# Kernel tuning notes

Measured on AMD Instinct MI355X. Metric: run time of the kernel, lower is better.

Reference implementation:

```python
import jax, jax.numpy as jnp
import numpy as np
from jax import lax

V, B, T, H = 16, 64, 256, 128  # num_variables, batch, seq_len, rnn_hidden_size
FC, C = 256, 10                # fc_hidden_size, num_classes


def setup_inputs() -> dict:
    key = jax.random.key(0)
    ks = jax.random.split(key, 8)
    s = 1.0 / np.sqrt(H)
    return {
        "x":   jax.random.normal(ks[0], (V, B, T, 1), jnp.float32),
        "Wih": jax.random.uniform(ks[1], (V, 3 * H, 1), jnp.float32, -s, s),
        "Whh": jax.random.uniform(ks[2], (V, 3 * H, H), jnp.float32, -s, s),
        "bih": jnp.zeros((V, 3 * H), jnp.float32),
        "bhh": jnp.zeros((V, 3 * H), jnp.float32),
        "Wp":  jax.random.normal(ks[3], (V, H), jnp.float32) * s,  # xavier-ish
        "bp":  jnp.zeros((V,), jnp.float32),
        "W1":  jax.random.normal(ks[4], (FC, V), jnp.float32) * (1.0 / np.sqrt(V)),
        "b1":  jnp.zeros((FC,), jnp.float32),
        "W2":  jax.random.normal(ks[5], (C, FC), jnp.float32) * (1.0 / np.sqrt(FC)),
        "b2":  jnp.zeros((C,), jnp.float32),
    }


def reference(x, Wih, Whh, bih, bhh, Wp, bp, W1, b1, W2, b2):
    # Batched multi-head GRU: all V independent heads scanned together.
    # Precompute input-side gates for all steps: [T, V, B, 3H]
    gi = jnp.einsum('vbti,vgi->tvbg', x, Wih) + bih[None, :, None, :]

    def step(h, gi_t):
        gh = jnp.einsum('vbh,vgh->vbg', h, Whh) + bhh[:, None, :]
        i_r, i_z, i_n = jnp.split(gi_t, 3, axis=-1)
        h_r, h_z, h_n = jnp.split(gh, 3, axis=-1)
        r = jax.nn.sigmoid(i_r + h_r)
        z = jax.nn.sigmoid(i_z + h_z)
        n = jnp.tanh(i_n + r * h_n)
        h_new = (1.0 - z) * n + z * h  # PyTorch GRU update
        return h_new, None

    h0 = jnp.zeros((x.shape[0], x.shape[1], Whh.shape[-1]), x.dtype)
    h_last, _ = lax.scan(step, h0, gi)  # [V, B, H] — last timestep hidden

    # per-variable Linear(H, 1), then concat over variables -> [B, V]
    concat = jnp.einsum('vbh,vh->bv', h_last, Wp) + bp[None, :]

    # Classifier: Linear -> ReLU -> Linear
    hfc = jax.nn.relu(concat @ W1.T + b1)
    return hfc @ W2.T + b2  # [B, C]
```

## Files before the change

### kernel.cpp

```cpp
#include <hip/hip_runtime.h>

#define NV  16
#define NB  64
#define NT  256
#define NH  128
#define NFC 256
#define NC  10

typedef _Float16 half8  __attribute__((ext_vector_type(8)));
typedef float    f32x4  __attribute__((ext_vector_type(4)));

__global__ __launch_bounds__(512, 2) void gru_scan_kernel(
    const float* __restrict__ x,   const float* __restrict__ Wih,
    const float* __restrict__ Whh, const float* __restrict__ bih,
    const float* __restrict__ bhh, const float* __restrict__ Wp,
    const float* __restrict__ bp,  float* __restrict__ concat_ws)
{
    __shared__ __align__(16) _Float16 frag[2][2048];
    __shared__ float xT[NT][5];
    __shared__ float pc[8][4];

    const int tid = threadIdx.x;
    const int w   = tid >> 6;
    const int l   = tid & 63;
    const int r   = l & 15;
    const int m4  = l >> 4;
    const int rb  = l & 3;
    const int s   = (l >> 2) & 3;
    const int bid = blockIdx.x;
    const int v   = bid >> 4;
    const int b0  = (bid & 15) << 2;
    const int j0  = (w << 4) + (m4 << 2);
    const int j   = j0 + s;

    constexpr float L2E = 1.44269504088896340736f;
    const float SCL0 = -L2E, SCL2 = 2.0f * L2E;

    {
        const int rr = tid >> 7;
        const int t0 = (tid & 127) << 1;
        const float2 xv = *(const float2*)(x + (size_t)(v * NB + b0 + rr) * NT + t0);
        xT[t0][rr] = xv.x; xT[t0 + 1][rr] = xv.y;
    }
    ((int4*)frag)[tid] = int4{0, 0, 0, 0};

    half8 afr[3][4];
    #pragma unroll
    for (int g = 0; g < 3; ++g) {
        const float sc = (g == 2) ? SCL2 : SCL0;
        #pragma unroll
        for (int kb = 0; kb < 4; ++kb) {
            const float* wpp = Whh + (size_t)(v * 384 + g * 128 + (w << 4) + r) * 128
                             + kb * 32 + m4 * 8;
            float4 lo = *(const float4*)wpp;
            float4 hi = *(const float4*)(wpp + 4);
            half8 hf;
            hf[0]=(_Float16)(sc*lo.x); hf[1]=(_Float16)(sc*lo.y);
            hf[2]=(_Float16)(sc*lo.z); hf[3]=(_Float16)(sc*lo.w);
            hf[4]=(_Float16)(sc*hi.x); hf[5]=(_Float16)(sc*hi.y);
            hf[6]=(_Float16)(sc*hi.z); hf[7]=(_Float16)(sc*hi.w);
            afr[g][kb] = hf;
        }
    }

    f32x4 c0i, c1i, c2i;
    #pragma unroll
    for (int q = 0; q < 4; ++q) {
        const int i0 = v * 384 + j0 + q;
        c0i[q] = SCL0 * (bhh[i0] + bih[i0]);
        c1i[q] = SCL0 * (bhh[i0 + 128] + bih[i0 + 128]);
        c2i[q] = SCL2 * bhh[i0 + 256];
    }
    const int ih = v * 384 + j;
    const float wih0 = SCL0 * Wih[ih];
    const float wih1 = SCL0 * Wih[ih + 128];
    const float wihn = SCL2 * Wih[ih + 256];
    const float bihn = SCL2 * bih[ih + 256];
    const float wpj  = Wp[v * NH + j];

    float h_old = 0.f;

    const int fwoff = (j >> 5) * 512 + (rb + 16 * ((j & 31) >> 3)) * 8 + (j & 7);
    const int rdoff = l * 8;

    __syncthreads();

    auto step = [&](const _Float16* __restrict__ fb, _Float16* __restrict__ fwb,
                    const float xr) {
        half8 bfr[4];
        #pragma unroll
        for (int kb = 0; kb < 4; ++kb)
            bfr[kb] = *(const half8*)(fb + kb * 512 + rdoff);

        f32x4 acc0 = __builtin_amdgcn_mfma_f32_16x16x32_f16(afr[0][0], bfr[0], c0i, 0, 0, 0);
        f32x4 acc1 = __builtin_amdgcn_mfma_f32_16x16x32_f16(afr[1][0], bfr[0], c1i, 0, 0, 0);
        f32x4 acc2 = __builtin_amdgcn_mfma_f32_16x16x32_f16(afr[2][0], bfr[0], c2i, 0, 0, 0);
        #pragma unroll
        for (int kb = 1; kb < 4; ++kb) {
            acc0 = __builtin_amdgcn_mfma_f32_16x16x32_f16(afr[0][kb], bfr[kb], acc0, 0, 0, 0);
            acc1 = __builtin_amdgcn_mfma_f32_16x16x32_f16(afr[1][kb], bfr[kb], acc1, 0, 0, 0);
            acc2 = __builtin_amdgcn_mfma_f32_16x16x32_f16(afr[2][kb], bfr[kb], acc2, 0, 0, 0);
        }

        const bool s1 = (s & 1) != 0, s2 = (s & 2) != 0;
        const float g0 = s2 ? (s1 ? acc0[3] : acc0[2]) : (s1 ? acc0[1] : acc0[0]);
        const float g1 = s2 ? (s1 ? acc1[3] : acc1[2]) : (s1 ? acc1[1] : acc1[0]);
        const float g2 = s2 ? (s1 ? acc2[3] : acc2[2]) : (s1 ? acc2[1] : acc2[0]);

        const float srs = fmaf(xr, wih0, g0);
        const float szs = fmaf(xr, wih1, g1);
        const float gns = fmaf(xr, wihn, bihn);
        const float rg  = __builtin_amdgcn_rcpf(1.f + __builtin_amdgcn_exp2f(srs));
        const float a   = __builtin_amdgcn_exp2f(szs);
        const float ccs = fmaf(rg, g2, gns);
        const float b   = __builtin_amdgcn_exp2f(-ccs);
        const float h   = h_old;
        const float num = fmaf(b, h - a, a + h);
        const float den = (1.f + a) * (1.f + b);
        const float hn  = num * __builtin_amdgcn_rcpf(den);
        h_old = hn;
        const _Float16 hv = (_Float16)hn;
        fwb[fwoff]      = hv;
        fwb[fwoff + 32] = hv;
        fwb[fwoff + 64] = hv;
        fwb[fwoff + 96] = hv;
        __syncthreads();
    };

    for (int t = 0; t < NT; t += 2) {
        const float xa = xT[t][rb];
        const float xb = xT[t + 1][rb];
        step(&frag[0][0], &frag[1][0], xa);
        step(&frag[1][0], &frag[0][0], xb);
    }

    float partial = h_old * wpj;
    partial += __shfl_xor(partial, 4, 64);
    partial += __shfl_xor(partial, 8, 64);
    partial += __shfl_xor(partial, 16, 64);
    partial += __shfl_xor(partial, 32, 64);
    if (l < 4) pc[w][l] = partial;
    __syncthreads();
    if (tid < 4) {
        float acc = bp[v];
        #pragma unroll
        for (int ww = 0; ww < 8; ++ww) acc += pc[ww][tid];
        concat_ws[(b0 + tid) * NV + v] = acc;
    }
}

__global__ __launch_bounds__(256, 1) void fc_kernel(
    const float* __restrict__ cws, const float* __restrict__ W1,
    const float* __restrict__ b1,  const float* __restrict__ W2,
    const float* __restrict__ b2,  float* __restrict__ out)
{
    __shared__ float cc[NB][NV + 1];
    __shared__ float hfc[NB][NFC + 1];
    const int tid = threadIdx.x;
    for (int i = tid; i < NB * NV; i += 256) cc[i >> 4][i & 15] = cws[i];
    __syncthreads();

    float w1r[NV];
    #pragma unroll
    for (int q = 0; q < NV; q += 4) {
        float4 t4 = *(const float4*)(W1 + tid * NV + q);
        w1r[q] = t4.x; w1r[q+1] = t4.y; w1r[q+2] = t4.z; w1r[q+3] = t4.w;
    }
    const float bb = b1[tid];
    for (int b = 0; b < NB; ++b) {
        float sacc = bb;
        #pragma unroll
        for (int q = 0; q < NV; ++q) sacc = fmaf(cc[b][q], w1r[q], sacc);
        hfc[b][tid] = fmaxf(sacc, 0.f);
    }
    __syncthreads();

    for (int idx = tid; idx < NB * NC; idx += 256) {
        const int b = idx / NC, c = idx % NC;
        const float* w2r = W2 + c * NFC;
        float sacc = b2[c];
        #pragma unroll 4
        for (int f = 0; f < NFC; f += 4) {
            float4 wv = *(const float4*)(w2r + f);
            sacc = fmaf(hfc[b][f+0], wv.x, sacc);
            sacc = fmaf(hfc[b][f+1], wv.y, sacc);
            sacc = fmaf(hfc[b][f+2], wv.z, sacc);
            sacc = fmaf(hfc[b][f+3], wv.w, sacc);
        }
        out[idx] = sacc;
    }
}

extern "C" void kernel_launch(void* const* d_in, const int* in_sizes, int n_in,
                              void* d_out, int out_size, void* d_ws, size_t ws_size,
                              hipStream_t stream) {
    const float* x   = (const float*)d_in[0];
    const float* Wih = (const float*)d_in[1];
    const float* Whh = (const float*)d_in[2];
    const float* bih = (const float*)d_in[3];
    const float* bhh = (const float*)d_in[4];
    const float* Wp  = (const float*)d_in[5];
    const float* bp  = (const float*)d_in[6];
    const float* W1  = (const float*)d_in[7];
    const float* b1  = (const float*)d_in[8];
    const float* W2  = (const float*)d_in[9];
    const float* b2  = (const float*)d_in[10];
    float* out = (float*)d_out;
    float* cws = (float*)d_ws;

    gru_scan_kernel<<<dim3(256), dim3(512), 0, stream>>>(x, Wih, Whh, bih, bhh, Wp, bp, cws);
    fc_kernel<<<dim3(1), dim3(256), 0, stream>>>(cws, W1, b1, W2, b2, out);
}
```

Before: 199.5 us.

## Interleave two independent batch groups per block to hide GRU step latency

Each block now processes 8 batch rows as two independent 4-row recurrences (A and B), interleaving their MFMA chains and gate math within one barrier per step. The grid drops from 256 to 128 blocks, which halves the number of blocks and gives each wave two independent dependency chains to overlap MFMA and transcendental latency. The cost is more registers and LDS per block and fewer blocks spread across the CUs, so fewer CUs may be busy.

Measured after the change: 267.6 us. 1.34x slower.

```diff
diff --git a/kernel.cpp b/kernel.cpp
--- a/kernel.cpp
+++ b/kernel.cpp
@@ -16,9 +16,10 @@
     const float* __restrict__ bhh, const float* __restrict__ Wp,
     const float* __restrict__ bp,  float* __restrict__ concat_ws)
 {
-    __shared__ __align__(16) _Float16 frag[2][2048];
-    __shared__ float xT[NT][5];
-    __shared__ float pc[8][4];
+    __shared__ __align__(16) _Float16 fragA[2][2048];
+    __shared__ __align__(16) _Float16 fragB[2][2048];
+    __shared__ float xT[NT][9];
+    __shared__ float pc[8][8];
 
     const int tid = threadIdx.x;
     const int w   = tid >> 6;
@@ -28,8 +29,8 @@
     const int rb  = l & 3;
     const int s   = (l >> 2) & 3;
     const int bid = blockIdx.x;
-    const int v   = bid >> 4;
-    const int b0  = (bid & 15) << 2;
+    const int v   = bid >> 3;
+    const int b0  = (bid & 7) << 3;
     const int j0  = (w << 4) + (m4 << 2);
     const int j   = j0 + s;
 
@@ -37,12 +38,13 @@
     const float SCL0 = -L2E, SCL2 = 2.0f * L2E;
 
     {
-        const int rr = tid >> 7;
-        const int t0 = (tid & 127) << 1;
-        const float2 xv = *(const float2*)(x + (size_t)(v * NB + b0 + rr) * NT + t0);
-        xT[t0][rr] = xv.x; xT[t0 + 1][rr] = xv.y;
-    }
-    ((int4*)frag)[tid] = int4{0, 0, 0, 0};
+        const int rr = tid >> 6;
+        const int t0 = (tid & 63) << 2;
+        const float4 xv = *(const float4*)(x + (size_t)(v * NB + b0 + rr) * NT + t0);
+        xT[t0][rr] = xv.x; xT[t0+1][rr] = xv.y; xT[t0+2][rr] = xv.z; xT[t0+3][rr] = xv.w;
+    }
+    ((int4*)fragA)[tid] = int4{0, 0, 0, 0};
+    ((int4*)fragB)[tid] = int4{0, 0, 0, 0};
 
     half8 afr[3][4];
     #pragma unroll
@@ -78,70 +80,94 @@
     const float bihn = SCL2 * bih[ih + 256];
     const float wpj  = Wp[v * NH + j];
 
-    float h_old = 0.f;
+    float h_oldA = 0.f, h_oldB = 0.f;
 
     const int fwoff = (j >> 5) * 512 + (rb + 16 * ((j & 31) >> 3)) * 8 + (j & 7);
     const int rdoff = l * 8;
 
     __syncthreads();
 
-    auto step = [&](const _Float16* __restrict__ fb, _Float16* __restrict__ fwb,
-                    const float xr) {
-        half8 bfr[4];
-        #pragma unroll
-        for (int kb = 0; kb < 4; ++kb)
-            bfr[kb] = *(const half8*)(fb + kb * 512 + rdoff);
-
-        f32x4 acc0 = __builtin_amdgcn_mfma_f32_16x16x32_f16(afr[0][0], bfr[0], c0i, 0, 0, 0);
-        f32x4 acc1 = __builtin_amdgcn_mfma_f32_16x16x32_f16(afr[1][0], bfr[0], c1i, 0, 0, 0);
-        f32x4 acc2 = __builtin_amdgcn_mfma_f32_16x16x32_f16(afr[2][0], bfr[0], c2i, 0, 0, 0);
+    auto period = [&](const _Float16* __restrict__ fbA, _Float16* __restrict__ fwA,
+                      const _Float16* __restrict__ fbB, _Float16* __restrict__ fwB,
+                      const float xrA, const float xrB) {
+        half8 bfrA[4], bfrB[4];
+        #pragma unroll
+        for (int kb = 0; kb < 4; ++kb) {
+            bfrA[kb] = *(const half8*)(fbA + kb * 512 + rdoff);
+            bfrB[kb] = *(const half8*)(fbB + kb * 512 + rdoff);
+        }
+
+        f32x4 aA0 = __builtin_amdgcn_mfma_f32_16x16x32_f16(afr[0][0], bfrA[0], c0i, 0, 0, 0);
+        f32x4 aA1 = __builtin_amdgcn_mfma_f32_16x16x32_f16(afr[1][0], bfrA[0], c1i, 0, 0, 0);
+        f32x4 aA2 = __builtin_amdgcn_mfma_f32_16x16x32_f16(afr[2][0], bfrA[0], c2i, 0, 0, 0);
+        f32x4 aB0 = __builtin_amdgcn_mfma_f32_16x16x32_f16(afr[0][0], bfrB[0], c0i, 0, 0, 0);
+        f32x4 aB1 = __builtin_amdgcn_mfma_f32_16x16x32_f16(afr[1][0], bfrB[0], c1i, 0, 0, 0);
+        f32x4 aB2 = __builtin_amdgcn_mfma_f32_16x16x32_f16(afr[2][0], bfrB[0], c2i, 0, 0, 0);
         #pragma unroll
         for (int kb = 1; kb < 4; ++kb) {
-            acc0 = __builtin_amdgcn_mfma_f32_16x16x32_f16(afr[0][kb], bfr[kb], acc0, 0, 0, 0);
-            acc1 = __builtin_amdgcn_mfma_f32_16x16x32_f16(afr[1][kb], bfr[kb], acc1, 0, 0, 0);
-            acc2 = __builtin_amdgcn_mfma_f32_16x16x32_f16(afr[2][kb], bfr[kb], acc2, 0, 0, 0);
+            aA0 = __builtin_amdgcn_mfma_f32_16x16x32_f16(afr[0][kb], bfrA[kb], aA0, 0, 0, 0);
+            aA1 = __builtin_amdgcn_mfma_f32_16x16x32_f16(afr[1][kb], bfrA[kb], aA1, 0, 0, 0);
+            aA2 = __builtin_amdgcn_mfma_f32_16x16x32_f16(afr[2][kb], bfrA[kb], aA2, 0, 0, 0);
+            aB0 = __builtin_amdgcn_mfma_f32_16x16x32_f16(afr[0][kb], bfrB[kb], aB0, 0, 0, 0);
+            aB1 = __builtin_amdgcn_mfma_f32_16x16x32_f16(afr[1][kb], bfrB[kb], aB1, 0, 0, 0);
+            aB2 = __builtin_amdgcn_mfma_f32_16x16x32_f16(afr[2][kb], bfrB[kb], aB2, 0, 0, 0);
         }
 
         const bool s1 = (s & 1) != 0, s2 = (s & 2) != 0;
-        const float g0 = s2 ? (s1 ? acc0[3] : acc0[2]) : (s1 ? acc0[1] : acc0[0]);
-        const float g1 = s2 ? (s1 ? acc1[3] : acc1[2]) : (s1 ? acc1[1] : acc1[0]);
-        const float g2 = s2 ? (s1 ? acc2[3] : acc2[2]) : (s1 ? acc2[1] : acc2[0]);
-
-        const float srs = fmaf(xr, wih0, g0);
-        const float szs = fmaf(xr, wih1, g1);
-        const float gns = fmaf(xr, wihn, bihn);
-        const float rg  = __builtin_amdgcn_rcpf(1.f + __builtin_amdgcn_exp2f(srs));
-        const float a   = __builtin_amdgcn_exp2f(szs);
-        const float ccs = fmaf(rg, g2, gns);
-        const float b   = __builtin_amdgcn_exp2f(-ccs);
-        const float h   = h_old;
-        const float num = fmaf(b, h - a, a + h);
-        const float den = (1.f + a) * (1.f + b);
-        const float hn  = num * __builtin_amdgcn_rcpf(den);
-        h_old = hn;
-        const _Float16 hv = (_Float16)hn;
-        fwb[fwoff]      = hv;
-        fwb[fwoff + 32] = hv;
-        fwb[fwoff + 64] = hv;
-        fwb[fwoff + 96] = hv;
+        const float gA0 = s2 ? (s1 ? aA0[3] : aA0[2]) : (s1 ? aA0[1] : aA0[0]);
+        const float gA1 = s2 ? (s1 ? aA1[3] : aA1[2]) : (s1 ? aA1[1] : aA1[0]);
+        const float gA2 = s2 ? (s1 ? aA2[3] : aA2[2]) : (s1 ? aA2[1] : aA2[0]);
+        const float gB0 = s2 ? (s1 ? aB0[3] : aB0[2]) : (s1 ? aB0[1] : aB0[0]);
+        const float gB1 = s2 ? (s1 ? aB1[3] : aB1[2]) : (s1 ? aB1[1] : aB1[0]);
+        const float gB2 = s2 ? (s1 ? aB2[3] : aB2[2]) : (s1 ? aB2[1] : aB2[0]);
+
+        const float srsA = fmaf(xrA, wih0, gA0);
+        const float szsA = fmaf(xrA, wih1, gA1);
+        const float gnsA = fmaf(xrA, wihn, bihn);
+        const float srsB = fmaf(xrB, wih0, gB0);
+        const float szsB = fmaf(xrB, wih1, gB1);
+        const float gnsB = fmaf(xrB, wihn, bihn);
+
+        const float rgA = __builtin_amdgcn_rcpf(1.f + __builtin_amdgcn_exp2f(srsA));
+        const float rgB = __builtin_amdgcn_rcpf(1.f + __builtin_amdgcn_exp2f(srsB));
+        const float aA  = __builtin_amdgcn_exp2f(szsA);
+        const float aB  = __builtin_amdgcn_exp2f(szsB);
+        const float ccA = fmaf(rgA, gA2, gnsA);
+        const float ccB = fmaf(rgB, gB2, gnsB);
+        const float bA  = __builtin_amdgcn_exp2f(-ccA);
+        const float bB  = __builtin_amdgcn_exp2f(-ccB);
+
+        const float numA = fmaf(bA, h_oldA - aA, aA + h_oldA);
+        const float numB = fmaf(bB, h_oldB - aB, aB + h_oldB);
+        const float denA = (1.f + aA) * (1.f + bA);
+        const float denB = (1.f + aB) * (1.f + bB);
+        const float hnA  = numA * __builtin_amdgcn_rcpf(denA);
+        const float hnB  = numB * __builtin_amdgcn_rcpf(denB);
+        h_oldA = hnA;
+        h_oldB = hnB;
+        const _Float16 hvA = (_Float16)hnA;
+        const _Float16 hvB = (_Float16)hnB;
+        fwA[fwoff]      = hvA;  fwB[fwoff]      = hvB;
+        fwA[fwoff + 32] = hvA;  fwB[fwoff + 32] = hvB;
+        fwA[fwoff + 64] = hvA;  fwB[fwoff + 64] = hvB;
+        fwA[fwoff + 96] = hvA;  fwB[fwoff + 96] = hvB;
         __syncthreads();
     };
 
     for (int t = 0; t < NT; t += 2) {
-        const float xa = xT[t][rb];
-        const float xb = xT[t + 1][rb];
-        step(&frag[0][0], &frag[1][0], xa);
-        step(&frag[1][0], &frag[0][0], xb);
-    }
-
-    float partial = h_old * wpj;
-    partial += __shfl_xor(partial, 4, 64);
-    partial += __shfl_xor(partial, 8, 64);
-    partial += __shfl_xor(partial, 16, 64);
-    partial += __shfl_xor(partial, 32, 64);
-    if (l < 4) pc[w][l] = partial;
-    __syncthreads();
-    if (tid < 4) {
+        period(fragA[0], fragA[1], fragB[0], fragB[1], xT[t][rb],     xT[t][4 + rb]);
+        period(fragA[1], fragA[0], fragB[1], fragB[0], xT[t + 1][rb], xT[t + 1][4 + rb]);
+    }
+
+    float pA = h_oldA * wpj;
+    float pB = h_oldB * wpj;
+    pA += __shfl_xor(pA, 4, 64);  pB += __shfl_xor(pB, 4, 64);
+    pA += __shfl_xor(pA, 8, 64);  pB += __shfl_xor(pB, 8, 64);
+    pA += __shfl_xor(pA, 16, 64); pB += __shfl_xor(pB, 16, 64);
+    pA += __shfl_xor(pA, 32, 64); pB += __shfl_xor(pB, 32, 64);
+    if (l < 4) { pc[w][l] = pA; pc[w][4 + l] = pB; }
+    __syncthreads();
+    if (tid < 8) {
         float acc = bp[v];
         #pragma unroll
         for (int ww = 0; ww < 8; ++ww) acc += pc[ww][tid];
@@ -208,6 +234,6 @@
     float* out = (float*)d_out;
     float* cws = (float*)d_ws;
 
-    gru_scan_kernel<<<dim3(256), dim3(512), 0, stream>>>(x, Wih, Whh, bih, bhh, Wp, bp, cws);
+    gru_scan_kernel<<<dim3(128), dim3(512), 0, stream>>>(x, Wih, Whh, bih, bhh, Wp, bp, cws);
     fc_kernel<<<dim3(1), dim3(256), 0, stream>>>(cws, W1, b1, W2, b2, out);
 }
```

## Split GRU scan into 2-batch blocks of 4 waves with two M-tiles per wave

Applied to the files above, without the earlier changes.

Restructures the GRU scan so each block handles 2 batch rows instead of 4, which doubles the grid to 512 blocks and halves the block to 256 threads. Each wave now owns 32 hidden units and issues 24 MFMAs per step instead of 12. The goal is more blocks across CUs and cheaper per-step __syncthreads with fewer waves. In exchange, register pressure roughly doubles for the weight fragments and accumulators, each step's MFMA chain gets longer, and the h broadcast to LDS is written 8 times instead of 4.

After: 261.7 us. 1.31x slower.

```diff
diff --git a/kernel.cpp b/kernel.cpp
--- a/kernel.cpp
+++ b/kernel.cpp
@@ -10,28 +10,29 @@
 typedef _Float16 half8  __attribute__((ext_vector_type(8)));
 typedef float    f32x4  __attribute__((ext_vector_type(4)));
 
-__global__ __launch_bounds__(512, 2) void gru_scan_kernel(
+__global__ __launch_bounds__(256, 2) void gru_scan_kernel(
     const float* __restrict__ x,   const float* __restrict__ Wih,
     const float* __restrict__ Whh, const float* __restrict__ bih,
     const float* __restrict__ bhh, const float* __restrict__ Wp,
     const float* __restrict__ bp,  float* __restrict__ concat_ws)
 {
     __shared__ __align__(16) _Float16 frag[2][2048];
-    __shared__ float xT[NT][5];
-    __shared__ float pc[8][4];
+    __shared__ float xT[NT][3];
+    __shared__ float pc[4][2];
 
     const int tid = threadIdx.x;
-    const int w   = tid >> 6;
+    const int w4  = tid >> 6;
     const int l   = tid & 63;
-    const int r   = l & 15;
+    const int n   = l & 15;
     const int m4  = l >> 4;
-    const int rb  = l & 3;
-    const int s   = (l >> 2) & 3;
+    const int rb  = n & 1;
+    const int s   = n >> 1;
+    const int q   = s & 3;
+    const int cr  = s >> 2;
     const int bid = blockIdx.x;
-    const int v   = bid >> 4;
-    const int b0  = (bid & 15) << 2;
-    const int j0  = (w << 4) + (m4 << 2);
-    const int j   = j0 + s;
+    const int v   = bid >> 5;
+    const int b0  = (bid & 31) << 1;
+    const int j   = (w4 << 5) + (cr << 4) + (m4 << 2) + q;
 
     constexpr float L2E = 1.44269504088896340736f;
     const float SCL0 = -L2E, SCL2 = 2.0f * L2E;
@@ -42,34 +43,46 @@
         const float2 xv = *(const float2*)(x + (size_t)(v * NB + b0 + rr) * NT + t0);
         xT[t0][rr] = xv.x; xT[t0 + 1][rr] = xv.y;
     }
-    ((int4*)frag)[tid] = int4{0, 0, 0, 0};
-
-    half8 afr[3][4];
+    ((int4*)frag)[tid]       = int4{0, 0, 0, 0};
+    ((int4*)frag)[tid + 256] = int4{0, 0, 0, 0};
+
+    half8 afr[3][2][4];
     #pragma unroll
     for (int g = 0; g < 3; ++g) {
         const float sc = (g == 2) ? SCL2 : SCL0;
         #pragma unroll
-        for (int kb = 0; kb < 4; ++kb) {
-            const float* wpp = Whh + (size_t)(v * 384 + g * 128 + (w << 4) + r) * 128
-                             + kb * 32 + m4 * 8;
-            float4 lo = *(const float4*)wpp;
-            float4 hi = *(const float4*)(wpp + 4);
-            half8 hf;
-            hf[0]=(_Float16)(sc*lo.x); hf[1]=(_Float16)(sc*lo.y);
-            hf[2]=(_Float16)(sc*lo.z); hf[3]=(_Float16)(sc*lo.w);
-            hf[4]=(_Float16)(sc*hi.x); hf[5]=(_Float16)(sc*hi.y);
-            hf[6]=(_Float16)(sc*hi.z); hf[7]=(_Float16)(sc*hi.w);
-            afr[g][kb] = hf;
-        }
-    }
-
-    f32x4 c0i, c1i, c2i;
+        for (int c2 = 0; c2 < 2; ++c2) {
+            #pragma unroll
+            for (int kb = 0; kb < 4; ++kb) {
+                const float* wpp = Whh
+                    + (size_t)(v * 384 + g * 128 + (w4 << 5) + (c2 << 4) + n) * 128
+                    + kb * 32 + m4 * 8;
+                float4 lo = *(const float4*)wpp;
+                float4 hi = *(const float4*)(wpp + 4);
+                half8 hf;
+                hf[0]=(_Float16)(sc*lo.x); hf[1]=(_Float16)(sc*lo.y);
+                hf[2]=(_Float16)(sc*lo.z); hf[3]=(_Float16)(sc*lo.w);
+                hf[4]=(_Float16)(sc*hi.x); hf[5]=(_Float16)(sc*hi.y);
+                hf[6]=(_Float16)(sc*hi.z); hf[7]=(_Float16)(sc*hi.w);
+                afr[g][c2][kb] = hf;
+            }
+        }
+    }
+
+    f32x4 cini[3][2];
     #pragma unroll
-    for (int q = 0; q < 4; ++q) {
-        const int i0 = v * 384 + j0 + q;
-        c0i[q] = SCL0 * (bhh[i0] + bih[i0]);
-        c1i[q] = SCL0 * (bhh[i0 + 128] + bih[i0 + 128]);
-        c2i[q] = SCL2 * bhh[i0 + 256];
+    for (int g = 0; g < 3; ++g) {
+        const float sc = (g == 2) ? SCL2 : SCL0;
+        #pragma unroll
+        for (int c2 = 0; c2 < 2; ++c2) {
+            #pragma unroll
+            for (int reg = 0; reg < 4; ++reg) {
+                const int i0 = v * 384 + g * 128 + (w4 << 5) + (c2 << 4) + (m4 << 2) + reg;
+                float bsum = bhh[i0];
+                if (g < 2) bsum += bih[i0];
+                cini[g][c2][reg] = sc * bsum;
+            }
+        }
     }
     const int ih = v * 384 + j;
     const float wih0 = SCL0 * Wih[ih];
@@ -80,7 +93,8 @@
 
     float h_old = 0.f;
 
-    const int fwoff = (j >> 5) * 512 + (rb + 16 * ((j & 31) >> 3)) * 8 + (j & 7);
+    const int fwbase = (w4 << 9) + (rb + 16 * ((cr << 1) + (m4 >> 1))) * 8
+                     + ((m4 & 1) << 2) + q;
     const int rdoff = l * 8;
 
     __syncthreads();
@@ -92,27 +106,36 @@
         for (int kb = 0; kb < 4; ++kb)
             bfr[kb] = *(const half8*)(fb + kb * 512 + rdoff);
 
-        f32x4 acc0 = __builtin_amdgcn_mfma_f32_16x16x32_f16(afr[0][0], bfr[0], c0i, 0, 0, 0);
-        f32x4 acc1 = __builtin_amdgcn_mfma_f32_16x16x32_f16(afr[1][0], bfr[0], c1i, 0, 0, 0);
-        f32x4 acc2 = __builtin_amdgcn_mfma_f32_16x16x32_f16(afr[2][0], bfr[0], c2i, 0, 0, 0);
-        #pragma unroll
-        for (int kb = 1; kb < 4; ++kb) {
-            acc0 = __builtin_amdgcn_mfma_f32_16x16x32_f16(afr[0][kb], bfr[kb], acc0, 0, 0, 0);
-            acc1 = __builtin_amdgcn_mfma_f32_16x16x32_f16(afr[1][kb], bfr[kb], acc1, 0, 0, 0);
-            acc2 = __builtin_amdgcn_mfma_f32_16x16x32_f16(afr[2][kb], bfr[kb], acc2, 0, 0, 0);
-        }
-
-        const bool s1 = (s & 1) != 0, s2 = (s & 2) != 0;
-        const float g0 = s2 ? (s1 ? acc0[3] : acc0[2]) : (s1 ? acc0[1] : acc0[0]);
-        const float g1 = s2 ? (s1 ? acc1[3] : acc1[2]) : (s1 ? acc1[1] : acc1[0]);
-        const float g2 = s2 ? (s1 ? acc2[3] : acc2[2]) : (s1 ? acc2[1] : acc2[0]);
-
-        const float srs = fmaf(xr, wih0, g0);
-        const float szs = fmaf(xr, wih1, g1);
+        f32x4 aa[3][2];
+        #pragma unroll
+        for (int g = 0; g < 3; ++g)
+            #pragma unroll
+            for (int c2 = 0; c2 < 2; ++c2)
+                aa[g][c2] = __builtin_amdgcn_mfma_f32_16x16x32_f16(
+                                afr[g][c2][0], bfr[0], cini[g][c2], 0, 0, 0);
+        #pragma unroll
+        for (int kb = 1; kb < 4; ++kb)
+            #pragma unroll
+            for (int g = 0; g < 3; ++g)
+                #pragma unroll
+                for (int c2 = 0; c2 < 2; ++c2)
+                    aa[g][c2] = __builtin_amdgcn_mfma_f32_16x16x32_f16(
+                                    afr[g][c2][kb], bfr[kb], aa[g][c2], 0, 0, 0);
+
+        const bool q1 = (q & 1) != 0, q2 = (q & 2) != 0;
+        float gv[3];
+        #pragma unroll
+        for (int g = 0; g < 3; ++g) {
+            const f32x4 t = cr ? aa[g][1] : aa[g][0];
+            gv[g] = q2 ? (q1 ? t[3] : t[2]) : (q1 ? t[1] : t[0]);
+        }
+
+        const float srs = fmaf(xr, wih0, gv[0]);
+        const float szs = fmaf(xr, wih1, gv[1]);
         const float gns = fmaf(xr, wihn, bihn);
         const float rg  = __builtin_amdgcn_rcpf(1.f + __builtin_amdgcn_exp2f(srs));
         const float a   = __builtin_amdgcn_exp2f(szs);
-        const float ccs = fmaf(rg, g2, gns);
+        const float ccs = fmaf(rg, gv[2], gns);
         const float b   = __builtin_amdgcn_exp2f(-ccs);
         const float h   = h_old;
         const float num = fmaf(b, h - a, a + h);
@@ -120,10 +143,9 @@
         const float hn  = num * __builtin_amdgcn_rcpf(den);
         h_old = hn;
         const _Float16 hv = (_Float16)hn;
-        fwb[fwoff]      = hv;
-        fwb[fwoff + 32] = hv;
-        fwb[fwoff + 64] = hv;
-        fwb[fwoff + 96] = hv;
+        #pragma unroll
+        for (int i = 0; i < 8; ++i)
+            fwb[fwbase + i * 16] = hv;
         __syncthreads();
     };
 
@@ -135,16 +157,17 @@
     }
 
     float partial = h_old * wpj;
+    partial += __shfl_xor(partial, 2, 64);
     partial += __shfl_xor(partial, 4, 64);
     partial += __shfl_xor(partial, 8, 64);
     partial += __shfl_xor(partial, 16, 64);
     partial += __shfl_xor(partial, 32, 64);
-    if (l < 4) pc[w][l] = partial;
-    __syncthreads();
-    if (tid < 4) {
+    if (l < 2) pc[w4][l] = partial;
+    __syncthreads();
+    if (tid < 2) {
         float acc = bp[v];
         #pragma unroll
-        for (int ww = 0; ww < 8; ++ww) acc += pc[ww][tid];
+        for (int ww = 0; ww < 4; ++ww) acc += pc[ww][tid];
         concat_ws[(b0 + tid) * NV + v] = acc;
     }
 }
@@ -208,6 +231,6 @@
     float* out = (float*)d_out;
     float* cws = (float*)d_ws;
 
-    gru_scan_kernel<<<dim3(256), dim3(512), 0, stream>>>(x, Wih, Whh, bih, bhh, Wp, bp, cws);
+    gru_scan_kernel<<<dim3(512), dim3(256), 0, stream>>>(x, Wih, Whh, bih, bhh, Wp, bp, cws);
     fc_kernel<<<dim3(1), dim3(256), 0, stream>>>(cws, W1, b1, W2, b2, out);
 }
```
